# Kernel optimization log

Measured on AMD Instinct MI355X. Metric: run time of the kernel, lower is better.

The kernel has to match this reference:

```python
import jax, jax.numpy as jnp
import numpy as np

N_USERS = 50000
N_ENT = 100000
N_NODES = N_USERS + N_ENT
N_EDGES = 2400000
EMB = 64
LAYER_DIMS = [(64, 64), (64, 32), (32, 16)]  # (in_dim, out_dim) per layer


def setup_inputs() -> dict:
    key = jax.random.key(0)
    ks = jax.random.split(key, 20)
    inp = {
        'user_embed': jax.random.normal(ks[0], (N_USERS, EMB), jnp.float32) * 0.1,
        'entity_embed': jax.random.normal(ks[1], (N_ENT, EMB), jnp.float32) * 0.1,
        'edge_val': jax.random.uniform(ks[2], (N_EDGES,), jnp.float32),
        'edge_row': jax.random.randint(ks[3], (N_EDGES,), 0, N_NODES),
        'edge_col': jax.random.randint(ks[4], (N_EDGES,), 0, N_NODES),
    }
    i = 5
    for k, (din, dout) in enumerate(LAYER_DIMS):
        scale = float(np.sqrt(6.0 / (din + dout)))  # xavier_uniform
        inp[f'W_gc_{k}'] = jax.random.uniform(ks[i], (din, dout), jnp.float32, -scale, scale); i += 1
        inp[f'b_gc_{k}'] = jnp.zeros((dout,), jnp.float32)
        inp[f'W_bi_{k}'] = jax.random.uniform(ks[i], (din, dout), jnp.float32, -scale, scale); i += 1
        inp[f'b_bi_{k}'] = jnp.zeros((dout,), jnp.float32)
    return inp


def _l2_normalize(x):
    # matches F.normalize(x, p=2, dim=1) with eps=1e-12
    return x / jnp.maximum(jnp.linalg.norm(x, axis=1, keepdims=True), 1e-12)


def reference(user_embed, entity_embed, edge_val, edge_row, edge_col,
              W_gc_0, b_gc_0, W_bi_0, b_bi_0,
              W_gc_1, b_gc_1, W_bi_1, b_bi_1,
              W_gc_2, b_gc_2, W_bi_2, b_bi_2):
    layers = [(W_gc_0, b_gc_0, W_bi_0, b_bi_0),
              (W_gc_1, b_gc_1, W_bi_1, b_bi_1),
              (W_gc_2, b_gc_2, W_bi_2, b_bi_2)]
    x = jnp.concatenate([user_embed, entity_embed], axis=0)  # [N, 64]
    all_emb = [x]
    for W_gc, b_gc, W_bi, b_bi in layers:
        # sparse A @ x : gather source features, scale by edge value, segment-sum into rows
        msgs = edge_val[:, None] * x[edge_col]                       # [E, d]
        side = jax.ops.segment_sum(msgs, edge_row, num_segments=N_NODES)  # [N, d]
        sum_emb = jax.nn.leaky_relu((x + side) @ W_gc + b_gc)        # GCN path
        bi_emb = jax.nn.leaky_relu((x * side) @ W_bi + b_bi)         # bi-interaction path
        x = _l2_normalize(sum_emb + bi_emb)                          # dropout p=0 (eval)
        all_emb.append(x)
    all_emb = jnp.concatenate(all_emb, axis=1)  # [N, 64+64+32+16]
    return all_emb[:N_USERS], all_emb[N_USERS:]
```

## Files before the change

### kernel.cpp

```cpp
#include <hip/hip_runtime.h>
#include <hip/hip_fp16.h>

constexpr int N_USERS = 50000;
constexpr int N_ENT   = 100000;
constexpr int N_NODES = 150000;
constexpr int N_EDGES = 2400000;
constexpr int OUT_D   = 176;

constexpr int NBKT      = 293;
constexpr int P1_BLOCKS = 293;
constexpr int CHUNK     = 8192;
constexpr int TBL       = NBKT * P1_BLOCKS;
constexpr int SCAN_BLKS = (TBL + 1023) / 1024;


typedef _Float16 h2v __attribute__((ext_vector_type(2)));
union H2U { unsigned u; h2v v; };

__device__ inline float dot2(unsigned a, unsigned b, float c) {
    H2U x, y; x.u = a; y.u = b;
    return __builtin_amdgcn_fdot2(x.v, y.v, c, false);
}

__global__ __launch_bounds__(256) void init_x_kernel(const float* __restrict__ ue,
                                                     const float* __restrict__ ee,
                                                     float* __restrict__ out,
                                                     __half* __restrict__ xh) {
    int tid = blockIdx.x * 256 + threadIdx.x;
    int n = tid >> 4, q = tid & 15;
    const float* src = (n < N_USERS) ? ue + (size_t)n * 64
                                     : ee + (size_t)(n - N_USERS) * 64;
    float4 v = *(const float4*)(src + q * 4);
    *(float4*)(out + (size_t)n * OUT_D + q * 4) = v;
    union { __half2 h[2]; uint2 u; } pk;
    pk.h[0] = __floats2half2_rn(v.x, v.y);
    pk.h[1] = __floats2half2_rn(v.z, v.w);
    *(uint2*)(xh + (size_t)n * 64 + q * 4) = pk.u;
}

__global__ __launch_bounds__(256) void conv_kernel(const float* __restrict__ src,
                                                   __half* __restrict__ xh, int DIN) {
    int tid = blockIdx.x * 256 + threadIdx.x;
    int n = tid / (DIN / 2), t = tid % (DIN / 2);
    float2 v = *(const float2*)(src + (size_t)n * OUT_D + 2 * t);
    *(__half2*)(xh + (size_t)n * DIN + 2 * t) = __floats2half2_rn(v.x, v.y);
}

__global__ __launch_bounds__(256) void wt_kernel(const float* __restrict__ Wg0,
                                                 const float* __restrict__ Wb0,
                                                 const float* __restrict__ Wg1,
                                                 const float* __restrict__ Wb1,
                                                 const float* __restrict__ Wg2,
                                                 const float* __restrict__ Wb2,
                                                 __half* __restrict__ WT) {
    int idx = blockIdx.x * 256 + threadIdx.x;
    const float* src; int dout, base;
    if (idx < 8192)       { base = (idx < 4096) ? 0 : 4096;
                            src  = (idx < 4096) ? Wg0 : Wb0;  dout = 64; }
    else if (idx < 12288) { base = (idx < 10240) ? 8192 : 10240;
                            src  = (idx < 10240) ? Wg1 : Wb1; dout = 32; }
    else                  { base = (idx < 12800) ? 12288 : 12800;
                            src  = (idx < 12800) ? Wg2 : Wb2; dout = 16; }
    int r = idx - base;
    int i = r / dout, o = r % dout;
    int dest = base + (i / 8) * dout * 8 + o * 8 + (i % 8);
    WT[dest] = __float2half(src[r]);
}

__global__ __launch_bounds__(256) void histP1_kernel(const int* __restrict__ er,
                                                     int* __restrict__ table) {
    __shared__ int h[NBKT];
    for (int i = threadIdx.x; i < NBKT; i += 256) h[i] = 0;
    __syncthreads();
    int base = blockIdx.x * CHUNK;
    for (int i = threadIdx.x; i < CHUNK; i += 256) {
        int e = base + i;
        if (e < N_EDGES) atomicAdd(&h[er[e] >> 9], 1);
    }
    __syncthreads();
    for (int i = threadIdx.x; i < NBKT; i += 256)
        table[i * P1_BLOCKS + blockIdx.x] = h[i];
}

__global__ __launch_bounds__(1024) void scanA_kernel(const int* __restrict__ a,
                                                     int* __restrict__ bsum, int n) {
    __shared__ int wsum[16];
    int i = blockIdx.x * 1024 + threadIdx.x;
    int v = (i < n) ? a[i] : 0;
    #pragma unroll
    for (int off = 32; off; off >>= 1) v += __shfl_xor(v, off);
    int lane = threadIdx.x & 63, w = threadIdx.x >> 6;
    if (lane == 0) wsum[w] = v;
    __syncthreads();
    if (threadIdx.x == 0) {
        int t = 0;
        #pragma unroll
        for (int k = 0; k < 16; ++k) t += wsum[k];
        bsum[blockIdx.x] = t;
    }
}

__global__ __launch_bounds__(1024) void scanB_kernel(int* __restrict__ bsum, int n) {
    __shared__ int wtot[16];
    __shared__ int carry_s;
    int tid = threadIdx.x;
    int lane = tid & 63, w = tid >> 6;
    if (tid == 0) carry_s = 0;
    __syncthreads();
    for (int base = 0; base < n; base += 1024) {
        int i = base + tid;
        int v = (i < n) ? bsum[i] : 0;
        int incl = v;
        #pragma unroll
        for (int off = 1; off < 64; off <<= 1) {
            int t = __shfl_up(incl, off);
            if (lane >= off) incl += t;
        }
        if (lane == 63) wtot[w] = incl;
        __syncthreads();
        int woff = 0, total = 0;
        #pragma unroll
        for (int k = 0; k < 16; ++k) {
            int tk = wtot[k];
            if (k < w) woff += tk;
            total += tk;
        }
        if (i < n) bsum[i] = carry_s + woff + incl - v;
        __syncthreads();
        if (tid == 0) carry_s += total;
        __syncthreads();
    }
}

__global__ __launch_bounds__(1024) void scanC_kernel(int* __restrict__ a,
                                                     const int* __restrict__ bsum, int n) {
    __shared__ int wtot[16];
    int i = blockIdx.x * 1024 + threadIdx.x;
    int lane = threadIdx.x & 63, w = threadIdx.x >> 6;
    int v = (i < n) ? a[i] : 0;
    int incl = v;
    #pragma unroll
    for (int off = 1; off < 64; off <<= 1) {
        int t = __shfl_up(incl, off);
        if (lane >= off) incl += t;
    }
    if (lane == 63) wtot[w] = incl;
    __syncthreads();
    int woff = 0;
    #pragma unroll
    for (int k = 0; k < 16; ++k) if (k < w) woff += wtot[k];
    if (i < n) a[i] = bsum[blockIdx.x] + woff + incl - v;
}

__global__ __launch_bounds__(256) void scatterP1_kernel(const float* __restrict__ ev,
                                                        const int*   __restrict__ er,
                                                        const int*   __restrict__ ec,
                                                        const int*   __restrict__ table,
                                                        unsigned long long* __restrict__ tmp) {
    __shared__ int lcur[NBKT];
    for (int i = threadIdx.x; i < NBKT; i += 256)
        lcur[i] = table[i * P1_BLOCKS + blockIdx.x];
    __syncthreads();
    int base = blockIdx.x * CHUNK;
    for (int i = threadIdx.x; i < CHUNK; i += 256) {
        int e = base + i;
        if (e < N_EDGES) {
            int r = er[e], c = ec[e];
            int v14 = (int)(ev[e] * 16384.0f + 0.5f);
            v14 = v14 > 16383 ? 16383 : v14;
            int pos = atomicAdd(&lcur[r >> 9], 1);
            tmp[pos] = ((unsigned long long)(r & 511) << 32)
                     | ((unsigned)c << 14) | (unsigned)v14;
        }
    }
}

__global__ __launch_bounds__(512) void pass2_kernel(const unsigned long long* __restrict__ tmp,
                                                    const int* __restrict__ table,
                                                    unsigned* __restrict__ edges,
                                                    int* __restrict__ cursor) {
    __shared__ int hcnt[512];
    __shared__ int sinc[512];
    __shared__ int lcur[512];
    int b = blockIdx.x;
    int tid = threadIdx.x;
    int eStart = table[b * P1_BLOCKS];
    int eEnd = (b + 1 < NBKT) ? table[(b + 1) * P1_BLOCKS] : N_EDGES;

    hcnt[tid] = 0;
    __syncthreads();
    for (int e = eStart + tid; e < eEnd; e += 512)
        atomicAdd(&hcnt[(int)(tmp[e] >> 32)], 1);
    __syncthreads();
    sinc[tid] = hcnt[tid];
    __syncthreads();
    #pragma unroll
    for (int off = 1; off < 512; off <<= 1) {
        int t = (tid >= off) ? sinc[tid - off] : 0;
        __syncthreads();
        sinc[tid] += t;
        __syncthreads();
    }
    int row = b * 512 + tid;
    if (row < N_NODES) cursor[row] = eStart + sinc[tid];
    lcur[tid] = eStart + sinc[tid] - hcnt[tid];
    __syncthreads();
    for (int e = eStart + tid; e < eEnd; e += 512) {
        unsigned long long rec = tmp[e];
        int pos = atomicAdd(&lcur[(int)(rec >> 32)], 1);
        edges[pos] = (unsigned)rec;
    }
}

template<int DIN, int DOUT>
__global__ __launch_bounds__(256, 4) void fused_layer_kernel(
        const int*          __restrict__ cursor,
        const unsigned int* __restrict__ edges,
        const __half*       __restrict__ xh,
        float* __restrict__ out,
        const __half* __restrict__ WT, int wgOff, int wbOff,
        const float* __restrict__ bgc, const float* __restrict__ bbi,
        int cin, int cout) {
    __shared__ unsigned ash[4][DIN / 2];
    __shared__ unsigned bsh[4][DIN / 2];

    int tid = threadIdx.x;
    int w = tid >> 6, lane = tid & 63;
    int n = blockIdx.x * 4 + w;

    constexpr int HP = DIN / 2;
    constexpr int NE = 128 / DIN;
    int g = lane / HP;
    int t = lane % HP;

    int s = n ? cursor[n - 1] : 0;
    int e_end = cursor[n];

    float2 xv = make_float2(0.f, 0.f);
    if (lane < HP) xv = *(const float2*)(out + (size_t)n * OUT_D + cin + 2 * lane);

    const __half2* xr = (const __half2*)xh;
    float accx = 0.f, accy = 0.f;

    for (int e = s; e < e_end; e += 8 * NE) {
        unsigned ue[8];
        #pragma unroll
        for (int j = 0; j < 8; ++j) {
            int i = e + j * NE + g;
            unsigned raw = edges[i];
            ue[j] = (i < e_end) ? raw : 0u;
        }
        float vv[8]; float2 f[8];
        #pragma unroll
        for (int j = 0; j < 8; ++j) {
            unsigned c = ue[j] >> 14;
            vv[j] = (float)(ue[j] & 16383u) * (1.0f / 16384.0f);
            f[j] = __half22float2(xr[(size_t)c * HP + t]);
        }
        #pragma unroll
        for (int j = 0; j < 8; ++j) {
            accx += vv[j] * f[j].x;
            accy += vv[j] * f[j].y;
        }
    }
    #pragma unroll
    for (int m = 32; m >= HP; m >>= 1) {
        accx += __shfl_xor(accx, m);
        accy += __shfl_xor(accy, m);
    }

    if (lane < HP) {
        __half2 a2 = __floats2half2_rn(xv.x + accx, xv.y + accy);
        __half2 b2 = __floats2half2_rn(xv.x * accx, xv.y * accy);
        ash[w][lane] = *(unsigned*)&a2;
        bsh[w][lane] = *(unsigned*)&b2;
    }
    __syncthreads();

    float hres = 0.f;
    if constexpr (DOUT == DIN) {
        int o = lane;
        uint4 wg[DIN / 8], wb[DIN / 8];
        #pragma unroll
        for (int k = 0; k < DIN / 8; ++k) {
            wg[k] = *(const uint4*)(WT + wgOff + (size_t)(k * DOUT + o) * 8);
            wb[k] = *(const uint4*)(WT + wbOff + (size_t)(k * DOUT + o) * 8);
        }
        float ag = bgc[o], ab = bbi[o];
        #pragma unroll
        for (int k = 0; k < DIN / 8; ++k) {
            uint4 a4 = *(const uint4*)&ash[w][k * 4];
            uint4 b4 = *(const uint4*)&bsh[w][k * 4];
            ag = dot2(a4.x, wg[k].x, ag); ag = dot2(a4.y, wg[k].y, ag);
            ag = dot2(a4.z, wg[k].z, ag); ag = dot2(a4.w, wg[k].w, ag);
            ab = dot2(b4.x, wb[k].x, ab); ab = dot2(b4.y, wb[k].y, ab);
            ab = dot2(b4.z, wb[k].z, ab); ab = dot2(b4.w, wb[k].w, ab);
        }
        ag = ag > 0.f ? ag : 0.01f * ag;
        ab = ab > 0.f ? ab : 0.01f * ab;
        hres = ag + ab;
    } else {
        int o = lane & (DOUT - 1);
        bool gc = lane < DOUT;
        bool active = lane < 2 * DOUT;
        int woff2 = gc ? wgOff : wbOff;
        uint4 wr[DIN / 8];
        #pragma unroll
        for (int k = 0; k < DIN / 8; ++k)
            wr[k] = *(const uint4*)(WT + woff2 + (size_t)(k * DOUT + o) * 8);
        const unsigned* sp = gc ? &ash[w][0] : &bsh[w][0];
        float own = active ? (gc ? bgc[o] : bbi[o]) : 0.f;
        #pragma unroll
        for (int k = 0; k < DIN / 8; ++k) {
            uint4 s4 = *(const uint4*)(sp + k * 4);
            own = dot2(s4.x, wr[k].x, own); own = dot2(s4.y, wr[k].y, own);
            own = dot2(s4.z, wr[k].z, own); own = dot2(s4.w, wr[k].w, own);
        }
        own = own > 0.f ? own : 0.01f * own;
        float other = __shfl_xor(own, DOUT);
        hres = own + other;
    }

    float hq = (lane < DOUT) ? hres : 0.f;
    float ss = hq * hq;
    #pragma unroll
    for (int off = 32; off; off >>= 1) ss += __shfl_xor(ss, off);

    if (lane < DOUT) {
        float inv = 1.f / fmaxf(sqrtf(ss), 1e-12f);
        out[(size_t)n * OUT_D + cout + lane] = hres * inv;
    }
}

extern "C" void kernel_launch(void* const* d_in, const int* in_sizes, int n_in,
                              void* d_out, int out_size, void* d_ws, size_t ws_size,
                              hipStream_t stream) {
    const float* ue = (const float*)d_in[0];
    const float* ee = (const float*)d_in[1];
    const float* ev = (const float*)d_in[2];
    const int*   er = (const int*)d_in[3];
    const int*   ec = (const int*)d_in[4];
    float* out = (float*)d_out;

    unsigned long long* tmp    = (unsigned long long*)d_ws;
    __half*             xh     = (__half*)d_ws;
    unsigned int*       edges  = (unsigned int*)((char*)d_ws + 19200000);
    int*                cursor = (int*)((char*)d_ws + 28800000);
    int*                table  = (int*)((char*)d_ws + 29400000);
    int*                bsum   = (int*)((char*)d_ws + 30000000);
    __half*             WT     = (__half*)((char*)d_ws + 30100000);

    histP1_kernel<<<P1_BLOCKS, 256, 0, stream>>>(er, table);
    scanA_kernel<<<SCAN_BLKS, 1024, 0, stream>>>(table, bsum, TBL);
    scanB_kernel<<<1, 1024, 0, stream>>>(bsum, SCAN_BLKS);
    scanC_kernel<<<SCAN_BLKS, 1024, 0, stream>>>(table, bsum, TBL);
    scatterP1_kernel<<<P1_BLOCKS, 256, 0, stream>>>(ev, er, ec, table, tmp);
    pass2_kernel<<<NBKT, 512, 0, stream>>>(tmp, table, edges, cursor);

    init_x_kernel<<<(N_NODES * 16) / 256, 256, 0, stream>>>(ue, ee, out, xh);
    wt_kernel<<<52, 256, 0, stream>>>((const float*)d_in[5],  (const float*)d_in[7],
                                      (const float*)d_in[9],  (const float*)d_in[11],
                                      (const float*)d_in[13], (const float*)d_in[15], WT);

    const int GRID = N_NODES / 4;

    fused_layer_kernel<64, 64><<<GRID, 256, 0, stream>>>(cursor, edges, xh, out,
        WT, 0, 4096, (const float*)d_in[6], (const float*)d_in[8], 0, 64);
    conv_kernel<<<(N_NODES * 32) / 256, 256, 0, stream>>>(out + 64, xh, 64);

    fused_layer_kernel<64, 32><<<GRID, 256, 0, stream>>>(cursor, edges, xh, out,
        WT, 8192, 10240, (const float*)d_in[10], (const float*)d_in[12], 64, 128);
    conv_kernel<<<(N_NODES * 16) / 256, 256, 0, stream>>>(out + 128, xh, 32);

    fused_layer_kernel<32, 16><<<GRID, 256, 0, stream>>>(cursor, edges, xh, out,
        WT, 12288, 12800, (const float*)d_in[14], (const float*)d_in[16], 128, 160);
}
```

Measured before the change: 374.8 us.

## Gather four halves per lane and accumulate edge messages with packed fp16 FMA

Edge values are now stored as a truncated fp16 bit pattern, so the aggregation kernel can rebuild a half directly from 14 bits with no int-to-float convert. Each lane now loads 8 bytes (four halves) per neighbour instead of four bytes, which halves the lanes needed per row and doubles the edges handled in parallel per wave. Products are accumulated with packed half2 FMAs and flushed to fp32 every four edges. This cuts ALU conversion work and widens the memory accesses, at the cost of lower precision in both the edge values and the partial sums.

```diff
diff --git a/kernel.cpp b/kernel.cpp
--- a/kernel.cpp
+++ b/kernel.cpp
@@ -166,11 +166,11 @@
         int e = base + i;
         if (e < N_EDGES) {
             int r = er[e], c = ec[e];
-            int v14 = (int)(ev[e] * 16384.0f + 0.5f);
-            v14 = v14 > 16383 ? 16383 : v14;
+            unsigned hb = (unsigned)__half_as_ushort(__float2half_rn(ev[e]));
+            unsigned v14 = (hb + 2u) >> 2;
             int pos = atomicAdd(&lcur[r >> 9], 1);
             tmp[pos] = ((unsigned long long)(r & 511) << 32)
-                     | ((unsigned)c << 14) | (unsigned)v14;
+                     | ((unsigned)c << 14) | v14;
         }
     }
 }
@@ -228,19 +228,19 @@
     int w = tid >> 6, lane = tid & 63;
     int n = blockIdx.x * 4 + w;
 
-    constexpr int HP = DIN / 2;
-    constexpr int NE = 128 / DIN;
-    int g = lane / HP;
-    int t = lane % HP;
+    constexpr int QP = DIN / 4;
+    constexpr int NE = 64 / QP;
+    int g = lane / QP;
+    int t = lane % QP;
 
     int s = n ? cursor[n - 1] : 0;
     int e_end = cursor[n];
 
-    float2 xv = make_float2(0.f, 0.f);
-    if (lane < HP) xv = *(const float2*)(out + (size_t)n * OUT_D + cin + 2 * lane);
-
-    const __half2* xr = (const __half2*)xh;
-    float accx = 0.f, accy = 0.f;
+    float4 xv = make_float4(0.f, 0.f, 0.f, 0.f);
+    if (lane < QP) xv = *(const float4*)(out + (size_t)n * OUT_D + cin + 4 * lane);
+
+    const uint2* xq = (const uint2*)xh;
+    float fx0 = 0.f, fx1 = 0.f, fx2 = 0.f, fx3 = 0.f;
 
     for (int e = s; e < e_end; e += 8 * NE) {
         unsigned ue[8];
@@ -250,30 +250,45 @@
             unsigned raw = edges[i];
             ue[j] = (i < e_end) ? raw : 0u;
         }
-        float vv[8]; float2 f[8];
+        uint2 xx[8];
+        #pragma unroll
+        for (int j = 0; j < 8; ++j)
+            xx[j] = xq[(size_t)(ue[j] >> 14) * QP + t];
+
+        __half2 a0 = __floats2half2_rn(0.f, 0.f);
+        __half2 a1 = a0;
         #pragma unroll
         for (int j = 0; j < 8; ++j) {
-            unsigned c = ue[j] >> 14;
-            vv[j] = (float)(ue[j] & 16383u) * (1.0f / 16384.0f);
-            f[j] = __half22float2(xr[(size_t)c * HP + t]);
-        }
-        #pragma unroll
-        for (int j = 0; j < 8; ++j) {
-            accx += vv[j] * f[j].x;
-            accy += vv[j] * f[j].y;
-        }
-    }
-    #pragma unroll
-    for (int m = 32; m >= HP; m >>= 1) {
-        accx += __shfl_xor(accx, m);
-        accy += __shfl_xor(accy, m);
-    }
-
-    if (lane < HP) {
-        __half2 a2 = __floats2half2_rn(xv.x + accx, xv.y + accy);
-        __half2 b2 = __floats2half2_rn(xv.x * accx, xv.y * accy);
-        ash[w][lane] = *(unsigned*)&a2;
-        bsh[w][lane] = *(unsigned*)&b2;
+            unsigned bits = (ue[j] & 0x3FFFu) << 2;
+            __half vh = __ushort_as_half((unsigned short)bits);
+            __half2 vv2 = __half2half2(vh);
+            a0 = __hfma2(vv2, *(__half2*)&xx[j].x, a0);
+            a1 = __hfma2(vv2, *(__half2*)&xx[j].y, a1);
+            if (j == 3 || j == 7) {
+                float2 f0 = __half22float2(a0);
+                float2 f1 = __half22float2(a1);
+                fx0 += f0.x; fx1 += f0.y; fx2 += f1.x; fx3 += f1.y;
+                a0 = __floats2half2_rn(0.f, 0.f); a1 = a0;
+            }
+        }
+    }
+    #pragma unroll
+    for (int m = 32; m >= QP; m >>= 1) {
+        fx0 += __shfl_xor(fx0, m);
+        fx1 += __shfl_xor(fx1, m);
+        fx2 += __shfl_xor(fx2, m);
+        fx3 += __shfl_xor(fx3, m);
+    }
+
+    if (lane < QP) {
+        __half2 a01 = __floats2half2_rn(xv.x + fx0, xv.y + fx1);
+        __half2 a23 = __floats2half2_rn(xv.z + fx2, xv.w + fx3);
+        __half2 b01 = __floats2half2_rn(xv.x * fx0, xv.y * fx1);
+        __half2 b23 = __floats2half2_rn(xv.z * fx2, xv.w * fx3);
+        ash[w][2 * lane]     = *(unsigned*)&a01;
+        ash[w][2 * lane + 1] = *(unsigned*)&a23;
+        bsh[w][2 * lane]     = *(unsigned*)&b01;
+        bsh[w][2 * lane + 1] = *(unsigned*)&b23;
     }
     __syncthreads();
 
```

New measurement: 401.3 us. 1.07x slower.
